# Kernel optimization log

Measured on AMD Instinct MI355X. Metric: run time of the kernel, lower is better.

The kernel has to match this reference:

```python
import jax, jax.numpy as jnp
import numpy as np

N = 50000   # num_node
E = 1600000 # edge_size (N * avg_degree 32)
B = 64      # batch, hardcoded via repeat(64,1,1) in the torch module


def setup_inputs() -> dict:
    key = jax.random.key(0)
    k = jax.random.split(key, 8)
    return {
        "t": jax.random.normal(k[0], (1,), dtype=jnp.float32),
        "input": jax.random.normal(k[1], (B, N), dtype=jnp.float32),
        "edge_i": jax.random.randint(k[2], (E,), 0, N, dtype=jnp.int32),
        "edge_j": jax.random.randint(k[3], (E,), 0, N, dtype=jnp.int32),
        "weight_react": jax.random.normal(k[4], (1, E), dtype=jnp.float32) / 10.0,
        "weight_diff": jax.random.normal(k[5], (1, E), dtype=jnp.float32) / 1000.0,
        "bias_reaction": jax.random.normal(k[6], (1, N), dtype=jnp.float32) / 10.0,
        "bias_diffusion": jax.random.normal(k[7], (1, N), dtype=jnp.float32) / 10.0,
    }


def _lap_matvec(x, w, src, dst, n):
    # W[src_e, dst_e] = w_e (duplicates coalesce by sum, as torch sparse_coo_tensor does)
    # L = diag(colsum(W)) - W ; returns x @ L^T applied batched: out[b, v] = (L x[b])[v]
    col = jax.ops.segment_sum(w, dst, num_segments=n)                 # [N] column sums
    msg = jax.ops.segment_sum(w[:, None] * x[:, dst].T, src,
                              num_segments=n)                          # [N, B]
    return col[None, :] * x - msg.T                                   # [B, N]


def reference(t, input, edge_i, edge_j, weight_react, weight_diff,
              bias_reaction, bias_diffusion):
    x = input                                                          # [B, N]
    n = x.shape[1]
    # reaction Laplacian uses edges (i -> j); diffusion uses transposed (j -> i)
    reaction = _lap_matvec(x, weight_react[0], edge_i, edge_j, n) + bias_reaction
    diffusion = _lap_matvec(x, weight_diff[0], edge_j, edge_i, n) + bias_diffusion
    # up and down both True: tanh(reaction) + diffusion + input
    return jnp.tanh(reaction) + diffusion + x
```

## Files before the change

kernel.cpp:

```cpp
#include <hip/hip_runtime.h>
#include <hip/hip_fp16.h>


#define BKT_SHIFT 7
#define BKT_NODES 128
#define HALF_NODES 64
#define RCAP 4608
#define CAP 80
#define CH 4096
#define NBP 512

#define RFL(x) __builtin_amdgcn_readfirstlane(x)

__device__ __forceinline__ unsigned bf16_rne(float f) {
    unsigned u = __float_as_uint(f);
    unsigned rb = (u >> 16) & 1u;
    u += 0x7FFFu + rb;
    return u >> 16;
}
__device__ __forceinline__ float bf16_lo(int y) {
    return __uint_as_float(((unsigned)y) << 16);
}
__device__ __forceinline__ float bf16_hi(int y) {
    return __uint_as_float((unsigned)y & 0xFFFF0000u);
}

__global__ void transpose_kernel(const float* __restrict__ x, __half* __restrict__ xth,
                                 int* __restrict__ gcur, int ngcur, int N) {
    __shared__ float tile[64][65];
    int v0 = blockIdx.x * 64;
    int tx = threadIdx.x;
    int ty = threadIdx.y;
    int flat = blockIdx.x * 1024 + ty * 64 + tx;
    if (flat < ngcur) gcur[flat] = 0;
    if (v0 + tx < N) {
        for (int b = ty; b < 64; b += 16)
            tile[tx][b] = x[b * N + v0 + tx];
    }
    __syncthreads();
    for (int vl = ty; vl < 64; vl += 16) {
        int v = v0 + vl;
        if (v < N)
            xth[(size_t)v * 64 + tx] = __float2half(tile[vl][tx]);
    }
}

__global__ void __launch_bounds__(512) partition_kernel(
        const int* __restrict__ ei, const int* __restrict__ ej,
        const float* __restrict__ wr, const float* __restrict__ wd,
        int* __restrict__ gcur, int2* __restrict__ runs,
        int E, int NB) {
    __shared__ int cnt[2 * NBP];
    __shared__ int base_a[2 * NBP];
    __shared__ int gb[2 * NBP];
    __shared__ int2 buf[2 * CH];

    int tid = threadIdx.x;
    int e0 = blockIdx.x * CH;
    int ch_len = min(CH, E - e0);
    if (ch_len <= 0) return;

    int my_i[8], my_j[8];
    unsigned my_w[8];
    #pragma unroll
    for (int k = 0; k < 8; ++k) {
        int t = tid + k * 512;
        if (t < ch_len) {
            int e = e0 + t;
            my_i[k] = ei[e];
            my_j[k] = ej[e];
            my_w[k] = (bf16_rne(wr[e]) << 16) | bf16_rne(wd[e]);
        } else {
            my_i[k] = -1;
        }
    }

    for (int b = tid; b < 2 * NBP; b += 512) cnt[b] = 0;
    __syncthreads();
    #pragma unroll
    for (int k = 0; k < 8; ++k) {
        if (my_i[k] >= 0) {
            atomicAdd(&cnt[my_i[k] >> BKT_SHIFT], 1);
            atomicAdd(&cnt[NBP + (my_j[k] >> BKT_SHIFT)], 1);
        }
    }
    __syncthreads();
    if (tid < 64) {
        int carry = 0;
        #pragma unroll
        for (int c = 0; c < (2 * NBP) / 64; ++c) {
            int idx = c * 64 + tid;
            int val = cnt[idx];
            int scan = val;
            for (int off = 1; off < 64; off <<= 1) {
                int n = __shfl_up(scan, off, 64);
                if (tid >= off) scan += n;
            }
            int excl = scan - val + carry;
            base_a[idx] = excl;
            cnt[idx] = excl;
            carry += __shfl(scan, 63, 64);
        }
    }
    __syncthreads();
    #pragma unroll
    for (int k = 0; k < 8; ++k) {
        if (my_i[k] >= 0) {
            int i = my_i[k], j = my_j[k];
            unsigned wv = my_w[k];
            int b0 = i >> BKT_SHIFT;
            int p0 = atomicAdd(&cnt[b0], 1);
            buf[p0] = make_int2((int)(((unsigned)b0 << 23) | ((unsigned)(i & 127) << 16) | (unsigned)j),
                                (int)wv);
            int b1 = j >> BKT_SHIFT;
            int p1 = atomicAdd(&cnt[NBP + b1], 1);
            buf[p1] = make_int2((int)(((unsigned)b1 << 23) | ((unsigned)(j & 127) << 16) | (unsigned)i),
                                (int)((wv << 16) | (wv >> 16)));
        }
    }
    __syncthreads();
    for (int cb = tid; cb < 2 * NBP; cb += 512) {
        int n = cnt[cb] - base_a[cb];
        if (n > 0) {
            int side = cb >> 9;
            int bkt = cb & (NBP - 1);
            gb[cb] = atomicAdd(&gcur[side * NB + bkt], n);
        }
    }
    __syncthreads();
    int total = 2 * ch_len;
    for (int t = tid; t < total; t += 512) {
        int2 p = buf[t];
        int side = (t >= ch_len) ? 1 : 0;
        int bkt = ((unsigned)p.x >> 23) & 0x1FF;
        int cb = side * NBP + bkt;
        int rank = gb[cb] + (t - base_a[cb]);
        if (rank < RCAP)
            runs[((size_t)(side * NB + bkt)) * RCAP + rank] = p;
    }
}

#define ACC8S(S0,S1,S2,S3,S4,S5,S6,S7, P, D)                              \
    {                                                                     \
        float wv_ = bf16_hi(P);                                           \
        float2 f_;                                                        \
        f_ = __half22float2(*(const __half2*)&(D).x);                     \
        S0 = fmaf(wv_, f_.x, S0); S1 = fmaf(wv_, f_.y, S1);               \
        f_ = __half22float2(*(const __half2*)&(D).y);                     \
        S2 = fmaf(wv_, f_.x, S2); S3 = fmaf(wv_, f_.y, S3);               \
        f_ = __half22float2(*(const __half2*)&(D).z);                     \
        S4 = fmaf(wv_, f_.x, S4); S5 = fmaf(wv_, f_.y, S5);               \
        f_ = __half22float2(*(const __half2*)&(D).w);                     \
        S6 = fmaf(wv_, f_.x, S6); S7 = fmaf(wv_, f_.y, S7);               \
    }

#define COMB3(A) { A += __shfl_xor(A, 8); A += __shfl_xor(A, 16); A += __shfl_xor(A, 32); }

#define CHUNK(PA0, PA1, PB0, PB1)                                         \
    {                                                                     \
        uint4 dA0 = xq[(((size_t)((unsigned)(PA0) & 0xFFFFu)) << 3) + bl];\
        uint4 dA1 = xq[(((size_t)((unsigned)(PA1) & 0xFFFFu)) << 3) + bl];\
        uint4 dB0 = xq[(((size_t)((unsigned)(PB0) & 0xFFFFu)) << 3) + bl];\
        uint4 dB1 = xq[(((size_t)((unsigned)(PB1) & 0xFFFFu)) << 3) + bl];\
        ACC8S(a0,a1,a2,a3,a4,a5,a6,a7, PA0, dA0)                          \
        ACC8S(a0,a1,a2,a3,a4,a5,a6,a7, PA1, dA1)                          \
        ACC8S(c0,c1,c2,c3,c4,c5,c6,c7, PB0, dB0)                          \
        ACC8S(c0,c1,c2,c3,c4,c5,c6,c7, PB1, dB1)                          \
    }

__global__ void __launch_bounds__(512, 8) sortgather_kernel(
        const int* __restrict__ gcur, const int2* __restrict__ runs,
        const __half* __restrict__ xth,
        __half* __restrict__ msg, float* __restrict__ colsum,
        int NB, int N) {
    __shared__ int cur[HALF_NODES];
    __shared__ float csum[HALF_NODES];
    __shared__ int dst[HALF_NODES * CAP];

    int blk = blockIdx.x;
    int sb = blk >> 1;
    int h  = blk & 1;
    int side = (sb >= NB) ? 1 : 0;
    int b = sb - side * NB;
    int v0 = (b << BKT_SHIFT) + h * HALF_NODES;
    int len = min(gcur[sb], RCAP);
    size_t roff = (size_t)sb * RCAP;
    int tid = threadIdx.x;

    int2 my[9];
    #pragma unroll
    for (int k = 0; k < 9; ++k) {
        int t = tid + k * 512;
        if (t < len) {
            long long raw = __builtin_nontemporal_load((const long long*)(runs + roff + t));
            my[k].x = (int)(unsigned)(raw & 0xFFFFFFFFll);
            my[k].y = (int)(unsigned)((unsigned long long)raw >> 32);
        } else my[k].x = -1;
    }

    if (tid < HALF_NODES) { cur[tid] = 0; csum[tid] = 0.f; }
    {
        int4* d4 = (int4*)dst;
        for (int idx = tid; idx < (HALF_NODES * CAP) / 4; idx += 512)
            d4[idx] = make_int4(0, 0, 0, 0);
    }
    __syncthreads();
    #pragma unroll
    for (int k = 0; k < 9; ++k) {
        if (my[k].x != -1) {
            int dl = ((unsigned)my[k].x >> 16) & 0x7F;
            if ((dl >> 6) == h) {
                int dll = dl & (HALF_NODES - 1);
                int pos = atomicAdd(&cur[dll], 1);
                if (pos < CAP)
                    dst[dll * CAP + pos] =
                        (int)(((unsigned)my[k].y & 0xFFFF0000u) | ((unsigned)my[k].x & 0xFFFFu));
                atomicAdd(&csum[dll], bf16_lo(my[k].y));
            }
        }
    }
    __syncthreads();

    const uint4* __restrict__ xq = (const uint4*)xth;
    int lane = tid & 63;
    int g  = lane >> 3;
    int bl = lane & 7;
    int wid = tid >> 6;
    for (int t = 0; t < HALF_NODES / 8; t += 2) {
        int dllA = wid * (HALF_NODES / 8) + t;
        int dllB = dllA + 1;
        int vA = v0 + dllA;
        int vB = v0 + dllB;
        const int* payA = dst + dllA * CAP + g;
        const int* payB = dst + dllB * CAP + g;
        int noct = RFL(max(min(cur[dllA], CAP), min(cur[dllB], CAP)) + 7) >> 3;
        int pA0 = payA[0],  pA1 = payA[8],  pA2 = payA[16], pA3 = payA[24];
        int pA4 = payA[32], pA5 = payA[40], pA6 = payA[48], pA7 = payA[56];
        int pA8 = payA[64], pA9 = payA[72];
        int pB0 = payB[0],  pB1 = payB[8],  pB2 = payB[16], pB3 = payB[24];
        int pB4 = payB[32], pB5 = payB[40], pB6 = payB[48], pB7 = payB[56];
        int pB8 = payB[64], pB9 = payB[72];
        float a0 = 0.f, a1 = 0.f, a2 = 0.f, a3 = 0.f;
        float a4 = 0.f, a5 = 0.f, a6 = 0.f, a7 = 0.f;
        float c0 = 0.f, c1 = 0.f, c2 = 0.f, c3 = 0.f;
        float c4 = 0.f, c5 = 0.f, c6 = 0.f, c7 = 0.f;
        CHUNK(pA0, pA1, pB0, pB1)
        if (noct > 2) CHUNK(pA2, pA3, pB2, pB3)
        if (noct > 4) CHUNK(pA4, pA5, pB4, pB5)
        if (noct > 6) CHUNK(pA6, pA7, pB6, pB7)
        if (noct > 8) CHUNK(pA8, pA9, pB8, pB9)
        COMB3(a0) COMB3(a1) COMB3(a2) COMB3(a3)
        COMB3(a4) COMB3(a5) COMB3(a6) COMB3(a7)
        COMB3(c0) COMB3(c1) COMB3(c2) COMB3(c3)
        COMB3(c4) COMB3(c5) COMB3(c6) COMB3(c7)
        if (vA < N && lane < 8) {
            __half2 h0 = __floats2half2_rn(a0, a1);
            __half2 h1 = __floats2half2_rn(a2, a3);
            __half2 h2 = __floats2half2_rn(a4, a5);
            __half2 h3 = __floats2half2_rn(a6, a7);
            uint4 st = make_uint4(*(unsigned*)&h0, *(unsigned*)&h1,
                                  *(unsigned*)&h2, *(unsigned*)&h3);
            *(uint4*)(msg + ((size_t)side * N + vA) * 64 + 8 * lane) = st;
        }
        if (vB < N && lane < 8) {
            __half2 h0 = __floats2half2_rn(c0, c1);
            __half2 h1 = __floats2half2_rn(c2, c3);
            __half2 h2 = __floats2half2_rn(c4, c5);
            __half2 h3 = __floats2half2_rn(c6, c7);
            uint4 st = make_uint4(*(unsigned*)&h0, *(unsigned*)&h1,
                                  *(unsigned*)&h2, *(unsigned*)&h3);
            *(uint4*)(msg + ((size_t)side * N + vB) * 64 + 8 * lane) = st;
        }
        if (lane == 0) {
            if (vA < N) colsum[(size_t)side * N + vA] = csum[dllA];
            if (vB < N) colsum[(size_t)side * N + vB] = csum[dllB];
        }
    }
}

__global__ void final_kernel(const float* __restrict__ x,
                             const __half* __restrict__ msg,
                             const float* __restrict__ colsum,
                             const float* __restrict__ br, const float* __restrict__ bd,
                             float* __restrict__ out, int N) {
    __shared__ float tr[64][65];
    __shared__ float td[64][65];
    int v0 = blockIdx.x * 64;
    int tx = threadIdx.x;
    int ty = threadIdx.y;
    for (int vl = ty; vl < 64; vl += 16) {
        int v = v0 + vl;
        if (v < N) {
            tr[vl][tx] = __half2float(msg[(size_t)v * 64 + tx]);
            td[vl][tx] = __half2float(msg[((size_t)N + v) * 64 + tx]);
        }
    }
    __syncthreads();
    int v = v0 + tx;
    if (v < N) {
        float cold = colsum[v];
        float colr = colsum[(size_t)N + v];
        float brv = br[v], bdv = bd[v];
        for (int b = ty; b < 64; b += 16) {
            float xv = x[b * N + v];
            float r = colr * xv - tr[tx][b] + brv;
            float d = cold * xv - td[tx][b] + bdv;
            out[b * N + v] = tanhf(r) + d + xv;
        }
    }
}

extern "C" void kernel_launch(void* const* d_in, const int* in_sizes, int n_in,
                              void* d_out, int out_size, void* d_ws, size_t ws_size,
                              hipStream_t stream) {
    const float* x  = (const float*)d_in[1];
    const int*   ei = (const int*)d_in[2];
    const int*   ej = (const int*)d_in[3];
    const float* wr = (const float*)d_in[4];
    const float* wd = (const float*)d_in[5];
    const float* br = (const float*)d_in[6];
    const float* bd = (const float*)d_in[7];
    float* out = (float*)d_out;

    int E = in_sizes[2];
    int N = in_sizes[6];
    int NB = (N + BKT_NODES - 1) >> BKT_SHIFT;
    (void)out_size; (void)ws_size; (void)n_in;

    char* w = (char*)d_ws;
    __half* xth = (__half*)w;    w += (size_t)N * 64 * 2;
    __half* msg = (__half*)w;    w += (size_t)2 * N * 64 * 2;
    float* colsum = (float*)w;   w += (size_t)2 * N * 4;
    int* gcur   = (int*)w;       w += (size_t)2 * NB * 4;
    w = (char*)(((uintptr_t)w + 15) & ~(uintptr_t)15);
    int2* runs  = (int2*)w;

    dim3 tb(64, 16);
    int ntiles = (N + 63) / 64;
    transpose_kernel<<<ntiles, tb, 0, stream>>>(x, xth, gcur, 2 * NB, N);

    int nchunks = (E + CH - 1) / CH;
    partition_kernel<<<nchunks, 512, 0, stream>>>(ei, ej, wr, wd, gcur, runs, E, NB);

    sortgather_kernel<<<4 * NB, 512, 0, stream>>>(gcur, runs, xth, msg, colsum, NB, N);

    final_kernel<<<ntiles, tb, 0, stream>>>(x, msg, colsum, br, bd, out, N);
}
```

Measured before the change: 194.4 us.

## Process four nodes per warp iteration in gather loop and vectorize final msg loads

```diff
diff --git a/kernel.cpp b/kernel.cpp
--- a/kernel.cpp
+++ b/kernel.cpp
@@ -9,8 +9,6 @@
 #define CAP 80
 #define CH 4096
 #define NBP 512
-
-#define RFL(x) __builtin_amdgcn_readfirstlane(x)
 
 __device__ __forceinline__ unsigned bf16_rne(float f) {
     unsigned u = __float_as_uint(f);
@@ -156,19 +154,18 @@
 
 #define COMB3(A) { A += __shfl_xor(A, 8); A += __shfl_xor(A, 16); A += __shfl_xor(A, 32); }
 
-#define CHUNK(PA0, PA1, PB0, PB1)                                         \
-    {                                                                     \
-        uint4 dA0 = xq[(((size_t)((unsigned)(PA0) & 0xFFFFu)) << 3) + bl];\
-        uint4 dA1 = xq[(((size_t)((unsigned)(PA1) & 0xFFFFu)) << 3) + bl];\
-        uint4 dB0 = xq[(((size_t)((unsigned)(PB0) & 0xFFFFu)) << 3) + bl];\
-        uint4 dB1 = xq[(((size_t)((unsigned)(PB1) & 0xFFFFu)) << 3) + bl];\
-        ACC8S(a0,a1,a2,a3,a4,a5,a6,a7, PA0, dA0)                          \
-        ACC8S(a0,a1,a2,a3,a4,a5,a6,a7, PA1, dA1)                          \
-        ACC8S(c0,c1,c2,c3,c4,c5,c6,c7, PB0, dB0)                          \
-        ACC8S(c0,c1,c2,c3,c4,c5,c6,c7, PB1, dB1)                          \
-    }
-
-__global__ void __launch_bounds__(512, 8) sortgather_kernel(
+#define STORE8(S0,S1,S2,S3,S4,S5,S6,S7, V)                                \
+    if ((V) < N && lane < 8) {                                            \
+        __half2 h0 = __floats2half2_rn(S0, S1);                           \
+        __half2 h1 = __floats2half2_rn(S2, S3);                           \
+        __half2 h2 = __floats2half2_rn(S4, S5);                           \
+        __half2 h3 = __floats2half2_rn(S6, S7);                           \
+        uint4 st = make_uint4(*(unsigned*)&h0, *(unsigned*)&h1,           \
+                              *(unsigned*)&h2, *(unsigned*)&h3);          \
+        *(uint4*)(msg + ((size_t)side * N + (V)) * 64 + 8 * lane) = st;   \
+    }
+
+__global__ void __launch_bounds__(512, 6) sortgather_kernel(
         const int* __restrict__ gcur, const int2* __restrict__ runs,
         const __half* __restrict__ xth,
         __half* __restrict__ msg, float* __restrict__ colsum,
@@ -226,54 +223,58 @@
     int g  = lane >> 3;
     int bl = lane & 7;
     int wid = tid >> 6;
-    for (int t = 0; t < HALF_NODES / 8; t += 2) {
+    for (int t = 0; t < HALF_NODES / 8; t += 4) {
         int dllA = wid * (HALF_NODES / 8) + t;
         int dllB = dllA + 1;
-        int vA = v0 + dllA;
-        int vB = v0 + dllB;
+        int dllC = dllA + 2;
+        int dllD = dllA + 3;
         const int* payA = dst + dllA * CAP + g;
         const int* payB = dst + dllB * CAP + g;
-        int noct = RFL(max(min(cur[dllA], CAP), min(cur[dllB], CAP)) + 7) >> 3;
-        int pA0 = payA[0],  pA1 = payA[8],  pA2 = payA[16], pA3 = payA[24];
-        int pA4 = payA[32], pA5 = payA[40], pA6 = payA[48], pA7 = payA[56];
-        int pA8 = payA[64], pA9 = payA[72];
-        int pB0 = payB[0],  pB1 = payB[8],  pB2 = payB[16], pB3 = payB[24];
-        int pB4 = payB[32], pB5 = payB[40], pB6 = payB[48], pB7 = payB[56];
-        int pB8 = payB[64], pB9 = payB[72];
+        const int* payC = dst + dllC * CAP + g;
+        const int* payD = dst + dllD * CAP + g;
+        int no = max(max(min(cur[dllA], CAP), min(cur[dllB], CAP)),
+                     max(min(cur[dllC], CAP), min(cur[dllD], CAP)));
+        int noct = (no + 7) >> 3;
         float a0 = 0.f, a1 = 0.f, a2 = 0.f, a3 = 0.f;
         float a4 = 0.f, a5 = 0.f, a6 = 0.f, a7 = 0.f;
         float c0 = 0.f, c1 = 0.f, c2 = 0.f, c3 = 0.f;
         float c4 = 0.f, c5 = 0.f, c6 = 0.f, c7 = 0.f;
-        CHUNK(pA0, pA1, pB0, pB1)
-        if (noct > 2) CHUNK(pA2, pA3, pB2, pB3)
-        if (noct > 4) CHUNK(pA4, pA5, pB4, pB5)
-        if (noct > 6) CHUNK(pA6, pA7, pB6, pB7)
-        if (noct > 8) CHUNK(pA8, pA9, pB8, pB9)
+        float e0 = 0.f, e1 = 0.f, e2 = 0.f, e3 = 0.f;
+        float e4 = 0.f, e5 = 0.f, e6 = 0.f, e7 = 0.f;
+        float f0 = 0.f, f1 = 0.f, f2 = 0.f, f3 = 0.f;
+        float f4 = 0.f, f5 = 0.f, f6 = 0.f, f7 = 0.f;
+        for (int o = 0; o < noct; ++o) {
+            int pA = payA[8 * o];
+            int pB = payB[8 * o];
+            int pC = payC[8 * o];
+            int pD = payD[8 * o];
+            uint4 dA = xq[(((size_t)((unsigned)pA & 0xFFFFu)) << 3) + bl];
+            uint4 dB = xq[(((size_t)((unsigned)pB & 0xFFFFu)) << 3) + bl];
+            uint4 dC = xq[(((size_t)((unsigned)pC & 0xFFFFu)) << 3) + bl];
+            uint4 dD = xq[(((size_t)((unsigned)pD & 0xFFFFu)) << 3) + bl];
+            ACC8S(a0,a1,a2,a3,a4,a5,a6,a7, pA, dA)
+            ACC8S(c0,c1,c2,c3,c4,c5,c6,c7, pB, dB)
+            ACC8S(e0,e1,e2,e3,e4,e5,e6,e7, pC, dC)
+            ACC8S(f0,f1,f2,f3,f4,f5,f6,f7, pD, dD)
+        }
         COMB3(a0) COMB3(a1) COMB3(a2) COMB3(a3)
         COMB3(a4) COMB3(a5) COMB3(a6) COMB3(a7)
         COMB3(c0) COMB3(c1) COMB3(c2) COMB3(c3)
         COMB3(c4) COMB3(c5) COMB3(c6) COMB3(c7)
-        if (vA < N && lane < 8) {
-            __half2 h0 = __floats2half2_rn(a0, a1);
-            __half2 h1 = __floats2half2_rn(a2, a3);
-            __half2 h2 = __floats2half2_rn(a4, a5);
-            __half2 h3 = __floats2half2_rn(a6, a7);
-            uint4 st = make_uint4(*(unsigned*)&h0, *(unsigned*)&h1,
-                                  *(unsigned*)&h2, *(unsigned*)&h3);
-            *(uint4*)(msg + ((size_t)side * N + vA) * 64 + 8 * lane) = st;
-        }
-        if (vB < N && lane < 8) {
-            __half2 h0 = __floats2half2_rn(c0, c1);
-            __half2 h1 = __floats2half2_rn(c2, c3);
-            __half2 h2 = __floats2half2_rn(c4, c5);
-            __half2 h3 = __floats2half2_rn(c6, c7);
-            uint4 st = make_uint4(*(unsigned*)&h0, *(unsigned*)&h1,
-                                  *(unsigned*)&h2, *(unsigned*)&h3);
-            *(uint4*)(msg + ((size_t)side * N + vB) * 64 + 8 * lane) = st;
-        }
+        COMB3(e0) COMB3(e1) COMB3(e2) COMB3(e3)
+        COMB3(e4) COMB3(e5) COMB3(e6) COMB3(e7)
+        COMB3(f0) COMB3(f1) COMB3(f2) COMB3(f3)
+        COMB3(f4) COMB3(f5) COMB3(f6) COMB3(f7)
+        int vA = v0 + dllA, vB = v0 + dllB, vC = v0 + dllC, vD = v0 + dllD;
+        STORE8(a0,a1,a2,a3,a4,a5,a6,a7, vA)
+        STORE8(c0,c1,c2,c3,c4,c5,c6,c7, vB)
+        STORE8(e0,e1,e2,e3,e4,e5,e6,e7, vC)
+        STORE8(f0,f1,f2,f3,f4,f5,f6,f7, vD)
         if (lane == 0) {
             if (vA < N) colsum[(size_t)side * N + vA] = csum[dllA];
             if (vB < N) colsum[(size_t)side * N + vB] = csum[dllB];
+            if (vC < N) colsum[(size_t)side * N + vC] = csum[dllC];
+            if (vD < N) colsum[(size_t)side * N + vD] = csum[dllD];
         }
     }
 }
@@ -288,11 +289,18 @@
     int v0 = blockIdx.x * 64;
     int tx = threadIdx.x;
     int ty = threadIdx.y;
-    for (int vl = ty; vl < 64; vl += 16) {
+    int flat = ty * 64 + tx;
+    int r = flat >> 5;
+    int p = flat & 31;
+    #pragma unroll
+    for (int pass = 0; pass < 2; ++pass) {
+        int vl = pass * 32 + r;
         int v = v0 + vl;
         if (v < N) {
-            tr[vl][tx] = __half2float(msg[(size_t)v * 64 + tx]);
-            td[vl][tx] = __half2float(msg[((size_t)N + v) * 64 + tx]);
+            float2 mr = __half22float2(*(const __half2*)(msg + (size_t)v * 64 + 2 * p));
+            float2 md = __half22float2(*(const __half2*)(msg + ((size_t)N + v) * 64 + 2 * p));
+            tr[vl][2 * p] = mr.x; tr[vl][2 * p + 1] = mr.y;
+            td[vl][2 * p] = md.x; td[vl][2 * p + 1] = md.y;
         }
     }
     __syncthreads();
@@ -303,9 +311,9 @@
         float brv = br[v], bdv = bd[v];
         for (int b = ty; b < 64; b += 16) {
             float xv = x[b * N + v];
-            float r = colr * xv - tr[tx][b] + brv;
-            float d = cold * xv - td[tx][b] + bdv;
-            out[b * N + v] = tanhf(r) + d + xv;
+            float r2 = colr * xv - tr[tx][b] + brv;
+            float d2 = cold * xv - td[tx][b] + bdv;
+            out[b * N + v] = tanhf(r2) + d2 + xv;
         }
     }
 }
```

Result: no change. 193.2 us (-0.6%).
